# Optimization experiments

Hardware: AMD Instinct MI355X
Metric: run time of the kernel (lower is better)

Reference implementation:

```python
import jax, jax.numpy as jnp
import numpy as np

RADIUS = 0.1
K = 32  # num_neighbors


def _ball_query(points, centers, radius, k):
    # points: [B,3,N], centers: [B,3,M] -> indices [B,M,K] (int32)
    # PVCNN semantics: first k point indices within radius of each center,
    # unfilled slots padded with the first in-ball index (0 if none in ball).
    N = points.shape[-1]
    p2 = jnp.sum(points * points, axis=1)            # [B,N]
    c2 = jnp.sum(centers * centers, axis=1)          # [B,M]
    cp = jnp.einsum('bdm,bdn->bmn', centers, points)  # [B,M,N]
    dist2 = c2[:, :, None] + p2[:, None, :] - 2.0 * cp
    valid = dist2 < radius * radius                  # [B,M,N]
    # score = point index if in ball else sentinel N; sorting ascending puts
    # the first k in-ball indices (in original point order) up front.
    scores = jnp.where(valid, jnp.arange(N, dtype=jnp.int32), jnp.int32(N))
    idx = jnp.sort(scores, axis=-1)[..., :k]         # [B,M,K]
    first = idx[..., :1]
    first = jnp.where(first == N, 0, first)          # no neighbor -> index 0
    return jnp.where(idx == N, first, idx)


def _group(feat, idx):
    # feat: [B,C,N], idx: [B,M,K] -> [B,C,M,K]
    return jnp.take_along_axis(feat[:, :, None, :], idx[:, None, :, :], axis=3)


def setup_inputs() -> dict:
    key = jax.random.key(0)
    k1, k2, k3 = jax.random.split(key, 3)
    B, N, M, C = 2, 16384, 4096, 32
    points_coords = jax.random.uniform(k1, (B, 3, N), dtype=jnp.float32)
    centers_coords = jax.random.uniform(k2, (B, 3, M), dtype=jnp.float32)
    points_features = jax.random.normal(k3, (B, C, N), dtype=jnp.float32)
    return {
        'points_coords': points_coords,
        'centers_coords': centers_coords,
        'points_features': points_features,
    }


def reference(points_coords, centers_coords, points_features):
    idx = _ball_query(points_coords, centers_coords, RADIUS, K)     # [B,M,K]
    nbr_coords = _group(points_coords, idx)                          # [B,3,M,K]
    nbr_coords = nbr_coords - centers_coords[:, :, :, None]         # relative
    nbr_feats = _group(points_features, idx)                         # [B,C,M,K]
    out = jnp.concatenate([nbr_coords, nbr_feats], axis=1)          # [B,3+C,M,K]
    return jnp.transpose(out, (0, 1, 3, 2))                          # [B,3+C,K,M]
```

## Files before the change

kernel.cpp:

```cpp
#include <hip/hip_runtime.h>

#define B_SZ  2
#define N_PTS 16384
#define M_CTR 4096
#define C_FT  32
#define K_NB  32
#define NCH   35
#define CH_STRIDE (K_NB * M_CTR)
#define CELLS 10
#define NCELL (CELLS * CELLS * CELLS)
#define NCHUNK 16

typedef float vfloat2 __attribute__((ext_vector_type(2)));

__device__ __forceinline__ float fmul(float a, float b) {
    float r; asm("v_mul_f32 %0, %1, %2" : "=v"(r) : "v"(a), "v"(b)); return r;
}
__device__ __forceinline__ float fadd(float a, float b) {
    float r; asm("v_add_f32 %0, %1, %2" : "=v"(r) : "v"(a), "v"(b)); return r;
}
__device__ __forceinline__ float fsub(float a, float b) {
    float r; asm("v_sub_f32 %0, %1, %2" : "=v"(r) : "v"(a), "v"(b)); return r;
}
__device__ __forceinline__ float ffma(float a, float b, float c) {
    float r; asm("v_fma_f32 %0, %1, %2, %3" : "=v"(r) : "v"(a), "v"(b), "v"(c));
    return r;
}

__device__ __forceinline__ bool bq_valid(float x, float y, float z,
                                         float cx, float cy, float cz,
                                         float c2, float r2) {
    const float p2 = fadd(fadd(fmul(x, x), fmul(y, y)), fmul(z, z));
    const float cp = ffma(cz, z, ffma(cy, y, fmul(cx, x)));
    return fsub(fadd(c2, p2), fmul(2.0f, cp)) < r2;
}

__device__ __forceinline__ int cell_of(float x, float y, float z) {
    int ci = (int)(x * 10.0f); ci = ci < 0 ? 0 : (ci > 9 ? 9 : ci);
    int cj = (int)(y * 10.0f); cj = cj < 0 ? 0 : (cj > 9 ? 9 : cj);
    int ck = (int)(z * 10.0f); ck = ck < 0 ? 0 : (ck > 9 ? 9 : ck);
    return (ck * CELLS + cj) * CELLS + ci;
}

__global__ __launch_bounds__(1024) void prep_kernel(
    const float* __restrict__ points,
    const float* __restrict__ feats,
    int* __restrict__ ghist,
    float* __restrict__ pf)
{
    __shared__ union {
        float tile[64][37];
        int   h[NCELL];
    } sh;
    const int t = threadIdx.x;

    if (blockIdx.x < 256) {
        const int jb = blockIdx.x >> 7;
        const int base_n = (blockIdx.x & 127) * 128;
#pragma unroll
        for (int half = 0; half < 2; ++half) {
            const int n0 = base_n + half * 64;
            if (half) __syncthreads();
            for (int i = t; i < NCH * 64; i += 1024) {
                const int r = i >> 6;
                const int c = i & 63;
                float v;
                if (r < 3) v = points[(jb * 3 + r) * N_PTS + n0 + c];
                else       v = feats[(jb * C_FT + (r - 3)) * N_PTS + n0 + c];
                sh.tile[c][r] = v;
            }
            if (t < 64) sh.tile[t][35] = 0.0f;
            __syncthreads();
            float* __restrict__ dst = pf + ((size_t)jb * N_PTS + n0) * 36;
            for (int o = t; o < 64 * 36; o += 1024) {
                const int c = o / 36;
                const int r = o - c * 36;
                dst[o] = sh.tile[c][r];
            }
        }
    } else {
        const int hb = blockIdx.x - 256;
        const int b = hb >> 4;
        const int q = hb & (NCHUNK - 1);
        for (int c = t; c < NCELL; c += 1024) sh.h[c] = 0;
        __syncthreads();
        const int n = q * 1024 + t;
        const float x = points[(b * 3 + 0) * N_PTS + n];
        const float y = points[(b * 3 + 1) * N_PTS + n];
        const float z = points[(b * 3 + 2) * N_PTS + n];
        atomicAdd(&sh.h[cell_of(x, y, z)], 1);
        __syncthreads();
        int* __restrict__ g = ghist + (b * NCHUNK + q) * NCELL;
        for (int c = t; c < NCELL; c += 1024) g[c] = sh.h[c];
    }
}

__global__ __launch_bounds__(256) void scatter_kernel(
    const float* __restrict__ points,
    const int* __restrict__ ghist,
    int* __restrict__ starts,
    float4* __restrict__ binned)
{
    const int t = threadIdx.x;
    const int lane = t & 63, wid = t >> 6;
    const int b = blockIdx.x >> 4;
    const int q = blockIdx.x & (NCHUNK - 1);

    __shared__ int curs[NCELL];
    __shared__ int wsum[4];

    const int c0 = 4 * t;
    int tot[4] = {0, 0, 0, 0};
    int pre[4] = {0, 0, 0, 0};
    if (c0 < NCELL) {
        const int* __restrict__ gb = ghist + b * NCHUNK * NCELL;
#pragma unroll
        for (int qq = 0; qq < NCHUNK; ++qq) {
            const int4 v = *(const int4*)&gb[qq * NCELL + c0];
            tot[0] += v.x; tot[1] += v.y; tot[2] += v.z; tot[3] += v.w;
            if (qq < q) { pre[0] += v.x; pre[1] += v.y;
                          pre[2] += v.z; pre[3] += v.w; }
        }
    }
    const int s = tot[0] + tot[1] + tot[2] + tot[3];
    int incl = s;
    for (int off = 1; off < 64; off <<= 1) {
        const int u = __shfl_up(incl, off);
        if (lane >= off) incl += u;
    }
    if (lane == 63) wsum[wid] = incl;
    __syncthreads();
    if (t == 0) {
        int acc = 0;
        for (int w2 = 0; w2 < 4; ++w2) {
            const int x = wsum[w2]; wsum[w2] = acc; acc += x;
        }
    }
    __syncthreads();
    if (c0 < NCELL) {
        int e = incl - s + wsum[wid];
#pragma unroll
        for (int i = 0; i < 4; ++i) {
            if (q == 0) starts[b * (NCELL + 1) + c0 + i] = e;
            curs[c0 + i] = e + pre[i];
            e += tot[i];
        }
        if (q == 0 && c0 + 4 == NCELL)
            starts[b * (NCELL + 1) + NCELL] = e;
    }
    __syncthreads();

    const float* __restrict__ px = points + (b * 3 + 0) * N_PTS;
    const float* __restrict__ py = points + (b * 3 + 1) * N_PTS;
    const float* __restrict__ pz = points + (b * 3 + 2) * N_PTS;
    float4* __restrict__ bb = binned + b * N_PTS;
#pragma unroll
    for (int i = 0; i < 4; ++i) {
        const int n = q * 1024 + i * 256 + t;
        const float x = px[n], y = py[n], z = pz[n];
        const int pos = atomicAdd(&curs[cell_of(x, y, z)], 1);
        bb[pos] = make_float4(x, y, z, __int_as_float(n));
    }
}

__global__ __launch_bounds__(256) void ball_query_kernel(
    const float4* __restrict__ binned,
    const float* __restrict__ centers,
    const int* __restrict__ starts,
    int* __restrict__ idx_out)
{
    const int lane = threadIdx.x & 63;
    const int wid  = threadIdx.x >> 6;
    const int cid  = blockIdx.x * 4 + wid;
    const int b = cid >> 12;
    const int m = cid & (M_CTR - 1);

    const float r2 = (float)(0.1 * 0.1);

    const float cx = centers[(b * 3 + 0) * M_CTR + m];
    const float cy = centers[(b * 3 + 1) * M_CTR + m];
    const float cz = centers[(b * 3 + 2) * M_CTR + m];
    const float c2 = fadd(fadd(fmul(cx, cx), fmul(cy, cy)), fmul(cz, cz));

    __shared__ unsigned bitmap[4][N_PTS / 32];
    unsigned* bm = bitmap[wid];
#pragma unroll
    for (int j = 0; j < 8; ++j) bm[j * 64 + lane] = 0u;

    int ci = (int)(cx * 10.0f); ci = ci < 0 ? 0 : (ci > 9 ? 9 : ci);
    int cj = (int)(cy * 10.0f); cj = cj < 0 ? 0 : (cj > 9 ? 9 : cj);
    int ck = (int)(cz * 10.0f); ck = ck < 0 ? 0 : (ck > 9 ? 9 : ck);
    ci = __builtin_amdgcn_readfirstlane(ci);
    cj = __builtin_amdgcn_readfirstlane(cj);
    ck = __builtin_amdgcn_readfirstlane(ck);
    const int i0 = ci > 0 ? ci - 1 : 0;
    const int i1 = ci < 9 ? ci + 1 : 9;
    const int* st = starts + b * (NCELL + 1);
    const float4* __restrict__ bp = binned + b * N_PTS;

    int lo_d[9], hi_d[9];
#pragma unroll
    for (int d = 0; d < 9; ++d) {
        const int jj = cj + (d % 3) - 1;
        const int kk = ck + (d / 3) - 1;
        const bool ok = (jj >= 0) & (jj <= 9) & (kk >= 0) & (kk <= 9);
        const int base = ok ? (kk * CELLS + jj) * CELLS : 0;
        const int lo = st[base + i0];
        const int hi = st[base + i1 + 1];
        lo_d[d] = ok ? lo : 0;
        hi_d[d] = ok ? hi : 0;
    }

#pragma unroll
    for (int d = 0; d < 9; ++d) {
        const int lo = lo_d[d];
        const int hi = hi_d[d];
        for (int s0 = lo; s0 < hi; s0 += 64) {
            const int t = s0 + lane;
            if (t < hi) {
                const float4 p = bp[t];
                if (bq_valid(p.x, p.y, p.z, cx, cy, cz, c2, r2)) {
                    const int n = __float_as_int(p.w);
                    atomicOr((int*)&bm[(((n >> 5) & 7) << 6) + (n >> 8)],
                             1 << (n & 31));
                }
            }
        }
    }

    unsigned w[8];
    int cnt = 0;
#pragma unroll
    for (int j = 0; j < 8; ++j) {
        w[j] = bm[j * 64 + lane];
        cnt += __popc(w[j]);
    }

    int incl = cnt;
    for (int off = 1; off < 64; off <<= 1) {
        const int v = __shfl_up(incl, off);
        if (lane >= off) incl += v;
    }
    const int total = __shfl(incl, 63);
    int slot = incl - cnt;

    int firstbit = 0x7fffffff;
#pragma unroll
    for (int j = 0; j < 8; ++j) {
        if (w[j] && firstbit == 0x7fffffff)
            firstbit = lane * 256 + j * 32 + (__ffs(w[j]) - 1);
    }
    for (int off = 32; off > 0; off >>= 1)
        firstbit = min(firstbit, __shfl_xor(firstbit, off));
    const int first_idx = (total == 0) ? 0 : firstbit;

    int* __restrict__ dst = idx_out + (b * K_NB) * M_CTR + m;
#pragma unroll
    for (int j = 0; j < 8; ++j) {
        unsigned x = w[j];
        while (x && slot < K_NB) {
            const int bit = __ffs(x) - 1;
            dst[slot * M_CTR] = lane * 256 + j * 32 + bit;
            x &= x - 1;
            ++slot;
        }
    }
    if (lane >= total && lane < K_NB) dst[lane * M_CTR] = first_idx;
}

__global__ __launch_bounds__(256) void gather_kernel(
    const float* __restrict__ pf,
    const float* __restrict__ centers,
    const int* __restrict__ idx,
    float* __restrict__ out)
{
    const int t = blockIdx.x * 256 + threadIdx.x;
    const int m = (t & (M_CTR / 2 - 1)) * 2;
    const int k = (t >> 11) & (K_NB - 1);
    const int b = t >> 16;

    const int2 nn = *(const int2*)&idx[(b * K_NB + k) * M_CTR + m];
    const float4* __restrict__ s0 =
        (const float4*)(pf + ((size_t)b * N_PTS + nn.x) * 36);
    const float4* __restrict__ s1 =
        (const float4*)(pf + ((size_t)b * N_PTS + nn.y) * 36);

    float4 f0[9], f1[9];
#pragma unroll
    for (int i = 0; i < 9; ++i) { f0[i] = s0[i]; f1[i] = s1[i]; }

    const float2 cx = *(const float2*)&centers[(b * 3 + 0) * M_CTR + m];
    const float2 cy = *(const float2*)&centers[(b * 3 + 1) * M_CTR + m];
    const float2 cz = *(const float2*)&centers[(b * 3 + 2) * M_CTR + m];

    float v0[36], v1[36];
#pragma unroll
    for (int i = 0; i < 9; ++i) {
        v0[4 * i + 0] = f0[i].x; v0[4 * i + 1] = f0[i].y;
        v0[4 * i + 2] = f0[i].z; v0[4 * i + 3] = f0[i].w;
        v1[4 * i + 0] = f1[i].x; v1[4 * i + 1] = f1[i].y;
        v1[4 * i + 2] = f1[i].z; v1[4 * i + 3] = f1[i].w;
    }
    v0[0] -= cx.x; v0[1] -= cy.x; v0[2] -= cz.x;
    v1[0] -= cx.y; v1[1] -= cy.y; v1[2] -= cz.y;

    float* __restrict__ o = out + ((size_t)b * NCH * K_NB + k) * M_CTR + m;
#pragma unroll
    for (int ch = 0; ch < NCH; ++ch) {
        vfloat2 pv; pv.x = v0[ch]; pv.y = v1[ch];
        __builtin_nontemporal_store(pv, (vfloat2*)&o[(size_t)ch * CH_STRIDE]);
    }
}

extern "C" void kernel_launch(void* const* d_in, const int* in_sizes, int n_in,
                              void* d_out, int out_size, void* d_ws, size_t ws_size,
                              hipStream_t stream) {
    const float* points  = (const float*)d_in[0];
    const float* centers = (const float*)d_in[1];
    const float* feats   = (const float*)d_in[2];
    float* out = (float*)d_out;

    char* ws = (char*)d_ws;
    int*    idx    = (int*)ws;
    float*  pf     = (float*)(ws + (1u << 20));
    int*    ghist  = (int*)(ws + 5636 * 1024);
    int*    starts = (int*)(ws + 5764 * 1024);
    float4* binned = (float4*)(ws + 5776 * 1024);

    prep_kernel<<<256 + B_SZ * NCHUNK, 1024, 0, stream>>>(
        points, feats, ghist, pf);
    scatter_kernel<<<B_SZ * NCHUNK, 256, 0, stream>>>(
        points, ghist, starts, binned);
    ball_query_kernel<<<(B_SZ * M_CTR) / 4, 256, 0, stream>>>(
        binned, centers, starts, idx);
    gather_kernel<<<(B_SZ * K_NB * M_CTR / 2) / 256, 256, 0, stream>>>(
        pf, centers, idx, out);
}
```

Measured before the change: 100.5 us.

## Move point-feature transpose from prep kernel into ball-query launch as extra blocks

The transpose of point coordinates and features into the interleaved pf layout moves out of the prep kernel and into additional blocks of the ball-query launch, sharing the shared-memory union with the bitmap. The prep kernel keeps only the histogram, so the short histogram, scatter and ball-query chain is no longer held back by the larger transpose work. The transpose now overlaps with ball-query compute. The trade-off is that the ball-query kernel's shared-memory footprint and register use may affect occupancy, and the transpose blocks are scheduled after the query blocks.

```diff
diff --git a/kernel.cpp b/kernel.cpp
--- a/kernel.cpp
+++ b/kernel.cpp
@@ -10,6 +10,8 @@
 #define CELLS 10
 #define NCELL (CELLS * CELLS * CELLS)
 #define NCHUNK 16
+#define BQ_BLOCKS ((B_SZ * M_CTR) / 4)
+#define TR_BLOCKS ((B_SZ * N_PTS) / 64)
 
 typedef float vfloat2 __attribute__((ext_vector_type(2)));
 
@@ -44,55 +46,22 @@
 
 __global__ __launch_bounds__(1024) void prep_kernel(
     const float* __restrict__ points,
-    const float* __restrict__ feats,
-    int* __restrict__ ghist,
-    float* __restrict__ pf)
+    int* __restrict__ ghist)
 {
-    __shared__ union {
-        float tile[64][37];
-        int   h[NCELL];
-    } sh;
+    __shared__ int h[NCELL];
     const int t = threadIdx.x;
-
-    if (blockIdx.x < 256) {
-        const int jb = blockIdx.x >> 7;
-        const int base_n = (blockIdx.x & 127) * 128;
-#pragma unroll
-        for (int half = 0; half < 2; ++half) {
-            const int n0 = base_n + half * 64;
-            if (half) __syncthreads();
-            for (int i = t; i < NCH * 64; i += 1024) {
-                const int r = i >> 6;
-                const int c = i & 63;
-                float v;
-                if (r < 3) v = points[(jb * 3 + r) * N_PTS + n0 + c];
-                else       v = feats[(jb * C_FT + (r - 3)) * N_PTS + n0 + c];
-                sh.tile[c][r] = v;
-            }
-            if (t < 64) sh.tile[t][35] = 0.0f;
-            __syncthreads();
-            float* __restrict__ dst = pf + ((size_t)jb * N_PTS + n0) * 36;
-            for (int o = t; o < 64 * 36; o += 1024) {
-                const int c = o / 36;
-                const int r = o - c * 36;
-                dst[o] = sh.tile[c][r];
-            }
-        }
-    } else {
-        const int hb = blockIdx.x - 256;
-        const int b = hb >> 4;
-        const int q = hb & (NCHUNK - 1);
-        for (int c = t; c < NCELL; c += 1024) sh.h[c] = 0;
-        __syncthreads();
-        const int n = q * 1024 + t;
-        const float x = points[(b * 3 + 0) * N_PTS + n];
-        const float y = points[(b * 3 + 1) * N_PTS + n];
-        const float z = points[(b * 3 + 2) * N_PTS + n];
-        atomicAdd(&sh.h[cell_of(x, y, z)], 1);
-        __syncthreads();
-        int* __restrict__ g = ghist + (b * NCHUNK + q) * NCELL;
-        for (int c = t; c < NCELL; c += 1024) g[c] = sh.h[c];
-    }
+    const int b = blockIdx.x >> 4;
+    const int q = blockIdx.x & (NCHUNK - 1);
+    for (int c = t; c < NCELL; c += 1024) h[c] = 0;
+    __syncthreads();
+    const int n = q * 1024 + t;
+    const float x = points[(b * 3 + 0) * N_PTS + n];
+    const float y = points[(b * 3 + 1) * N_PTS + n];
+    const float z = points[(b * 3 + 2) * N_PTS + n];
+    atomicAdd(&h[cell_of(x, y, z)], 1);
+    __syncthreads();
+    int* __restrict__ g = ghist + (b * NCHUNK + q) * NCELL;
+    for (int c = t; c < NCELL; c += 1024) g[c] = h[c];
 }
 
 __global__ __launch_bounds__(256) void scatter_kernel(
@@ -167,10 +136,42 @@
     const float4* __restrict__ binned,
     const float* __restrict__ centers,
     const int* __restrict__ starts,
+    const float* __restrict__ points,
+    const float* __restrict__ feats,
+    float* __restrict__ pf,
     int* __restrict__ idx_out)
 {
-    const int lane = threadIdx.x & 63;
-    const int wid  = threadIdx.x >> 6;
+    __shared__ union {
+        unsigned bitmap[4][N_PTS / 32];
+        float    tile[64][37];
+    } sh;
+    const int t = threadIdx.x;
+
+    if (blockIdx.x >= BQ_BLOCKS) {
+        const int tid = blockIdx.x - BQ_BLOCKS;
+        const int jb = tid >> 8;
+        const int n0 = (tid & 255) * 64;
+        for (int i = t; i < NCH * 64; i += 256) {
+            const int r = i >> 6;
+            const int c = i & 63;
+            float v;
+            if (r < 3) v = points[(jb * 3 + r) * N_PTS + n0 + c];
+            else       v = feats[(jb * C_FT + (r - 3)) * N_PTS + n0 + c];
+            sh.tile[c][r] = v;
+        }
+        if (t < 64) sh.tile[t][35] = 0.0f;
+        __syncthreads();
+        float* __restrict__ dst = pf + ((size_t)jb * N_PTS + n0) * 36;
+        for (int o = t; o < 64 * 36; o += 256) {
+            const int c = o / 36;
+            const int r = o - c * 36;
+            dst[o] = sh.tile[c][r];
+        }
+        return;
+    }
+
+    const int lane = t & 63;
+    const int wid  = t >> 6;
     const int cid  = blockIdx.x * 4 + wid;
     const int b = cid >> 12;
     const int m = cid & (M_CTR - 1);
@@ -182,8 +183,7 @@
     const float cz = centers[(b * 3 + 2) * M_CTR + m];
     const float c2 = fadd(fadd(fmul(cx, cx), fmul(cy, cy)), fmul(cz, cz));
 
-    __shared__ unsigned bitmap[4][N_PTS / 32];
-    unsigned* bm = bitmap[wid];
+    unsigned* bm = sh.bitmap[wid];
 #pragma unroll
     for (int j = 0; j < 8; ++j) bm[j * 64 + lane] = 0u;
 
@@ -216,9 +216,9 @@
         const int lo = lo_d[d];
         const int hi = hi_d[d];
         for (int s0 = lo; s0 < hi; s0 += 64) {
-            const int t = s0 + lane;
-            if (t < hi) {
-                const float4 p = bp[t];
+            const int tt = s0 + lane;
+            if (tt < hi) {
+                const float4 p = bp[tt];
                 if (bq_valid(p.x, p.y, p.z, cx, cy, cz, c2, r2)) {
                     const int n = __float_as_int(p.w);
                     atomicOr((int*)&bm[(((n >> 5) & 7) << 6) + (n >> 8)],
@@ -327,12 +327,11 @@
     int*    starts = (int*)(ws + 5764 * 1024);
     float4* binned = (float4*)(ws + 5776 * 1024);
 
-    prep_kernel<<<256 + B_SZ * NCHUNK, 1024, 0, stream>>>(
-        points, feats, ghist, pf);
+    prep_kernel<<<B_SZ * NCHUNK, 1024, 0, stream>>>(points, ghist);
     scatter_kernel<<<B_SZ * NCHUNK, 256, 0, stream>>>(
         points, ghist, starts, binned);
-    ball_query_kernel<<<(B_SZ * M_CTR) / 4, 256, 0, stream>>>(
-        binned, centers, starts, idx);
+    ball_query_kernel<<<BQ_BLOCKS + TR_BLOCKS, 256, 0, stream>>>(
+        binned, centers, starts, points, feats, pf, idx);
     gather_kernel<<<(B_SZ * K_NB * M_CTR / 2) / 256, 256, 0, stream>>>(
         pf, centers, idx, out);
 }
```

Result: no change. 99.76 us (median of 3 runs) (-0.7%).
